# Optimization experiments

Hardware: AMD Instinct MI355X
Metric: run time of the kernel (lower is better)

## Reference

```python
import jax, jax.numpy as jnp
import numpy as np

N = 100000   # nodes
E = 640000   # edges (before self-loops)
G = 1000     # graphs in batch
D_IN = 100
D = 128
EPS = 1e-5


def setup_inputs() -> dict:
    key = jax.random.key(0)
    ks = jax.random.split(key, 12)
    x = jax.random.normal(ks[0], (N, D_IN), dtype=jnp.float32)
    edge_index = jax.random.randint(ks[1], (2, E), 0, N, dtype=jnp.int64)
    edge_weight = jax.random.uniform(ks[2], (E,), dtype=jnp.float32)
    batch = jnp.sort(jax.random.randint(ks[3], (N,), 0, G, dtype=jnp.int64))
    def glorot(k, shape):
        fan = shape[0]
        return jax.random.normal(k, shape, dtype=jnp.float32) / np.float32(np.sqrt(fan))
    return {
        "x": x, "edge_index": edge_index, "edge_weight": edge_weight, "batch": batch,
        "W0": glorot(ks[4], (D_IN, D)), "b0": jnp.zeros((D,), jnp.float32),
        "W1": glorot(ks[5], (D, D)),    "b1": jnp.zeros((D,), jnp.float32),
        "W2": glorot(ks[6], (D, D)),    "b2": jnp.zeros((D,), jnp.float32),
        "gamma": jnp.ones((3, D), jnp.float32), "beta": jnp.zeros((3, D), jnp.float32),
        "run_mean": jnp.zeros((3, D), jnp.float32), "run_var": jnp.ones((3, D), jnp.float32),
        "Wout": glorot(ks[7], (D, 1)), "bout": jnp.zeros((1,), jnp.float32),
    }


def reference(x, edge_index, edge_weight, batch, W0, b0, W1, b1, W2, b2,
              gamma, beta, run_mean, run_var, Wout, bout):
    n = x.shape[0]
    # add self-loops with weight 1 (GCNConv default)
    loop = jnp.arange(n, dtype=edge_index.dtype)
    src = jnp.concatenate([edge_index[0], loop])
    dst = jnp.concatenate([edge_index[1], loop])
    ew = jnp.concatenate([edge_weight, jnp.ones((n,), edge_weight.dtype)])
    # symmetric normalization: D^{-1/2} A D^{-1/2}
    deg = jax.ops.segment_sum(ew, dst, num_segments=n)
    dinv = jnp.where(deg > 0, jax.lax.rsqrt(deg), 0.0)
    norm = dinv[src] * ew * dinv[dst]            # [E+N]

    def gcn_bn_relu(h, W, b, g, bt, rm, rv):
        h = h @ W                                 # linear first (cheaper gather dim)
        agg = jax.ops.segment_sum(h[src] * norm[:, None], dst, num_segments=n)
        agg = agg + b
        # BatchNorm1d in eval mode (running stats); dropout is identity in eval
        agg = g * (agg - rm) * jax.lax.rsqrt(rv + EPS) + bt
        return jax.nn.relu(agg)

    h = gcn_bn_relu(x, W0, b0, gamma[0], beta[0], run_mean[0], run_var[0])
    h = gcn_bn_relu(h, W1, b1, gamma[1], beta[1], run_mean[1], run_var[1])
    h = gcn_bn_relu(h, W2, b2, gamma[2], beta[2], run_mean[2], run_var[2])

    # global mean pool over graphs
    counts = jax.ops.segment_sum(jnp.ones((n,), h.dtype), batch, num_segments=G)
    pooled = jax.ops.segment_sum(h, batch, num_segments=G) / jnp.maximum(counts, 1.0)[:, None]
    return pooled @ Wout + bout
```

## Files before the change

### kernel.cpp

```cpp
#include <hip/hip_runtime.h>

#define BN_EPS 1e-5f
#define BINCAP 32

static inline size_t align_up(size_t x, size_t a) { return (x + a - 1) & ~(a - 1); }

typedef __attribute__((ext_vector_type(8))) short bf16x8;
typedef __attribute__((ext_vector_type(4))) float f32x4;

__device__ __forceinline__ void bf16split(float v, unsigned short& hi, unsigned short& lo) {
    unsigned u = __float_as_uint(v);
    unsigned rh = (u + 0x7FFFu + ((u >> 16) & 1u)) >> 16;
    float fh = __uint_as_float(rh << 16);
    hi = (unsigned short)rh;
    float rem = v - fh;
    unsigned u2 = __float_as_uint(rem);
    lo = (unsigned short)((u2 + 0x7FFFu + ((u2 >> 16) & 1u)) >> 16);
}

__device__ __forceinline__ unsigned short bf16rne(float v) {
    unsigned u = __float_as_uint(v);
    return (unsigned short)((u + 0x7FFFu + ((u >> 16) & 1u)) >> 16);
}

__device__ __forceinline__ float bf16f(unsigned h) { return __uint_as_float(h << 16); }
__device__ __forceinline__ float chlo(unsigned u) { return __uint_as_float(u << 16); }
__device__ __forceinline__ float chhi(unsigned u) { return __uint_as_float(u & 0xffff0000u); }


__global__ void place_kernel(const int* __restrict__ src, const int* __restrict__ dst,
                             const float* __restrict__ ew,
                             int* __restrict__ cntc, float* __restrict__ degf,
                             int2* __restrict__ bins, int E) {
    int e = blockIdx.x * blockDim.x + threadIdx.x;
    if (e >= E) return;
    int d = dst[e];
    float w = ew[e];
    int pos = atomicAdd(&cntc[d], 1);
    atomicAdd(&degf[d], w);
    if (pos < BINCAP)
        bins[(size_t)d * BINCAP + pos] = make_int2(src[e], __float_as_int(w));
}


__global__ void deginv_kernel(const float* __restrict__ degf,
                              float* __restrict__ dinv, int N) {
    int i = blockIdx.x * blockDim.x + threadIdx.x;
    if (i >= N) return;
    dinv[i] = rsqrtf(degf[i] + 1.0f);
}


__global__ void normfix_kernel(const int* __restrict__ cntc, int2* __restrict__ bins,
                               const float* __restrict__ dinv, int N) {
    int i = blockIdx.x * blockDim.x + threadIdx.x;
    if (i >= N) return;
    int cnt = cntc[i]; if (cnt > BINCAP) cnt = BINCAP;
    float di = dinv[i];
    int2* b = bins + (size_t)i * BINCAP;
    for (int j = 0; j < cnt; ++j) {
        int2 pr = b[j];
        float w = __int_as_float(pr.y) * dinv[pr.x] * di;
        b[j].y = __float_as_int(w);
    }
}


__global__ void convw_kernel(const float* __restrict__ W0, const float* __restrict__ W1,
                             const float* __restrict__ W2, int K0,
                             unsigned short* __restrict__ Whi, unsigned short* __restrict__ Wlo) {
    int idx = blockIdx.x * blockDim.x + threadIdx.x;
    if (idx >= 3 * 32 * 64 * 8) return;
    int j    = idx & 7;
    int lane = (idx >> 3) & 63;
    int f    = (idx >> 9) & 31;
    int l    = idx >> 14;
    int ct = f >> 2, k0c = f & 3;
    int quad = lane >> 4, m16 = lane & 15;
    int n = ct * 16 + m16;
    int k = k0c * 32 + quad * 8 + j;
    const float* W = (l == 0) ? W0 : (l == 1) ? W1 : W2;
    int Kl = (l == 0) ? K0 : 128;
    float v = (k < Kl) ? W[(size_t)k * 128 + n] : 0.f;
    unsigned short hi, lo;
    bf16split(v, hi, lo);
    Whi[idx] = hi;
    Wlo[idx] = lo;
}


__device__ __forceinline__ void mfma_tail(const bf16x8 ah[4], const bf16x8 al[4],
                                          const unsigned short* __restrict__ Whi,
                                          const unsigned short* __restrict__ Wlo,
                                          unsigned short* __restrict__ Yh,
                                          int row0, int quad, int m16, int lane, int N) {
    const bf16x8* Wh8 = (const bf16x8*)Whi;
    const bf16x8* Wl8 = (const bf16x8*)Wlo;

    f32x4 acc[8];
    #pragma unroll
    for (int ct = 0; ct < 8; ++ct) acc[ct] = (f32x4){0.f, 0.f, 0.f, 0.f};

    bf16x8 bh[2][4], bl[2][4];
    #pragma unroll
    for (int k0c = 0; k0c < 4; ++k0c) {
        bh[0][k0c] = Wh8[k0c * 64 + lane];
        bl[0][k0c] = Wl8[k0c * 64 + lane];
    }

    __builtin_amdgcn_s_setprio(1);
    #pragma unroll
    for (int ct = 0; ct < 8; ++ct) {
        int cur = ct & 1, nxt = cur ^ 1;
        if (ct < 7) {
            #pragma unroll
            for (int k0c = 0; k0c < 4; ++k0c) {
                bh[nxt][k0c] = Wh8[((ct + 1) * 4 + k0c) * 64 + lane];
                bl[nxt][k0c] = Wl8[((ct + 1) * 4 + k0c) * 64 + lane];
            }
        }
        #pragma unroll
        for (int k0c = 0; k0c < 4; ++k0c) {
            acc[ct] = __builtin_amdgcn_mfma_f32_16x16x32_bf16(ah[k0c], bh[cur][k0c], acc[ct], 0, 0, 0);
            acc[ct] = __builtin_amdgcn_mfma_f32_16x16x32_bf16(ah[k0c], bl[cur][k0c], acc[ct], 0, 0, 0);
            acc[ct] = __builtin_amdgcn_mfma_f32_16x16x32_bf16(al[k0c], bh[cur][k0c], acc[ct], 0, 0, 0);
        }
    }
    __builtin_amdgcn_s_setprio(0);

    #pragma unroll
    for (int ct = 0; ct < 8; ++ct) {
        #pragma unroll
        for (int rg = 0; rg < 4; ++rg) {
            int row = row0 + quad * 4 + rg;
            if (row < N)
                Yh[(size_t)row * 128 + ct * 16 + m16] = bf16rne(acc[ct][rg]);
        }
    }
}


__launch_bounds__(256, 2)
__global__ void gemm0_fused_kernel(const float* __restrict__ x, int D_IN,
                                   const unsigned short* __restrict__ Whi,
                                   const unsigned short* __restrict__ Wlo,
                                   unsigned short* __restrict__ Yh, int N) {
    int tid = threadIdx.x;
    int wid = tid >> 6, lane = tid & 63;
    int quad = lane >> 4, m16 = lane & 15;
    int row0 = blockIdx.x * 64 + wid * 16;

    int arow = row0 + m16;
    if (arow > N - 1) arow = N - 1;
    const float* xr = x + (size_t)arow * D_IN;

    bf16x8 ah[4], al[4];
    #pragma unroll
    for (int k0c = 0; k0c < 4; ++k0c) {
        int kb = k0c * 32 + quad * 8;
        float vs[8];
        if (kb + 8 <= D_IN) {
            float4 v0 = *((const float4*)(xr + kb));
            float4 v1 = *((const float4*)(xr + kb + 4));
            vs[0] = v0.x; vs[1] = v0.y; vs[2] = v0.z; vs[3] = v0.w;
            vs[4] = v1.x; vs[5] = v1.y; vs[6] = v1.z; vs[7] = v1.w;
        } else {
            #pragma unroll
            for (int j = 0; j < 8; ++j) vs[j] = (kb + j < D_IN) ? xr[kb + j] : 0.f;
        }
        #pragma unroll
        for (int j = 0; j < 8; ++j) {
            unsigned short hi, lo;
            bf16split(vs[j], hi, lo);
            ah[k0c][j] = (short)hi;
            al[k0c][j] = (short)lo;
        }
    }

    mfma_tail(ah, al, Whi, Wlo, Yh, row0, quad, m16, lane, N);
}


__global__ void scaleshift_kernel(const float* __restrict__ gamma, const float* __restrict__ beta,
                                  const float* __restrict__ rm, const float* __restrict__ rv,
                                  const float* __restrict__ b0, const float* __restrict__ b1,
                                  const float* __restrict__ b2,
                                  float* __restrict__ scale, float* __restrict__ shift) {
    int t = threadIdx.x;
    int l = t >> 7, j = t & 127;
    const float* bs = (l == 0) ? b0 : (l == 1) ? b1 : b2;
    float sc = gamma[t] * rsqrtf(rv[t] + BN_EPS);
    scale[t] = sc;
    shift[t] = beta[t] + (bs[j] - rm[t]) * sc;
}


__device__ __forceinline__ void gather_quad(const unsigned* __restrict__ Yh32,
                                            const int2* pr, const int* mq, int lane,
                                            float* ax, float* ay) {
    int mr = mq[0];
    if (mq[1] > mr) mr = mq[1];
    if (mq[2] > mr) mr = mq[2];
    if (mq[3] > mr) mr = mq[3];
    mr = (mr + 7) & ~7;
    for (int j = 0; j < mr; j += 8) {
        int s[4][8];
        float w[4][8];
        #pragma unroll
        for (int q = 0; q < 4; ++q) {
            #pragma unroll
            for (int t = 0; t < 8; ++t)
                s[q][t] = __builtin_amdgcn_readlane(pr[q].x, j + t);
        }
        unsigned u[4][8];
        #pragma unroll
        for (int q = 0; q < 4; ++q) {
            #pragma unroll
            for (int t = 0; t < 8; ++t)
                u[q][t] = Yh32[(size_t)s[q][t] * 64 + lane];
        }
        #pragma unroll
        for (int q = 0; q < 4; ++q) {
            #pragma unroll
            for (int t = 0; t < 8; ++t)
                w[q][t] = __int_as_float(__builtin_amdgcn_readlane(pr[q].y, j + t));
        }
        #pragma unroll
        for (int q = 0; q < 4; ++q) {
            #pragma unroll
            for (int t = 0; t < 8; ++t) {
                ax[q] += chlo(u[q][t]) * w[q][t];
                ay[q] += chhi(u[q][t]) * w[q][t];
            }
        }
    }
}


__launch_bounds__(64, 4)
__global__ void fused_agg_gemm_kernel(
        const unsigned* __restrict__ Yh_in,
        const int2* __restrict__ bins, const int* __restrict__ cntc,
        const float* __restrict__ dinv,
        const float* __restrict__ scale, const float* __restrict__ shift,
        const unsigned short* __restrict__ Whi, const unsigned short* __restrict__ Wlo,
        unsigned short* __restrict__ Yh_out, int N) {
    __shared__ float sA[16 * 132];
    int lane = threadIdx.x;
    int quad = lane >> 4, m16 = lane & 15;
    int row0 = blockIdx.x * 16;

    float2 sc = ((const float2*)scale)[lane];
    float2 sh = ((const float2*)shift)[lane];

    int mm[16]; float dv[16]; unsigned uh[16]; int2 gg[16];
    #pragma unroll
    for (int i = 0; i < 16; ++i) {
        int n = row0 + i; if (n > N - 1) n = N - 1;
        mm[i] = cntc[n];
        dv[i] = dinv[n];
        uh[i] = Yh_in[(size_t)n * 64 + lane];
    }
    #pragma unroll
    for (int i = 0; i < 16; ++i) {
        int n = row0 + i; if (n > N - 1) n = N - 1;
        int m = mm[i]; if (m > BINCAP) m = BINCAP;
        mm[i] = m;
        gg[i] = (lane < m) ? bins[(size_t)n * BINCAP + lane] : make_int2(n, 0);
    }

    #pragma unroll
    for (int b = 0; b < 16; b += 4) {
        float ax[4], ay[4];
        #pragma unroll
        for (int q = 0; q < 4; ++q) {
            float w0 = dv[b + q] * dv[b + q];
            ax[q] = chlo(uh[b + q]) * w0;
            ay[q] = chhi(uh[b + q]) * w0;
        }
        gather_quad(Yh_in, &gg[b], &mm[b], lane, ax, ay);
        #pragma unroll
        for (int q = 0; q < 4; ++q) {
            float ox = fmaxf(ax[q] * sc.x + sh.x, 0.f);
            float oy = fmaxf(ay[q] * sc.y + sh.y, 0.f);
            *((float2*)&sA[(b + q) * 132 + 2 * lane]) = make_float2(ox, oy);
        }
    }

    asm volatile("s_waitcnt lgkmcnt(0)" ::: "memory");
    __builtin_amdgcn_sched_barrier(0);

    bf16x8 ah[4], al[4];
    #pragma unroll
    for (int k0c = 0; k0c < 4; ++k0c) {
        float4 v0 = *((const float4*)&sA[m16 * 132 + k0c * 32 + quad * 8]);
        float4 v1 = *((const float4*)&sA[m16 * 132 + k0c * 32 + quad * 8 + 4]);
        float vs[8] = {v0.x, v0.y, v0.z, v0.w, v1.x, v1.y, v1.z, v1.w};
        #pragma unroll
        for (int j = 0; j < 8; ++j) {
            unsigned short hi, lo;
            bf16split(vs[j], hi, lo);
            ah[k0c][j] = (short)hi;
            al[k0c][j] = (short)lo;
        }
    }

    mfma_tail(ah, al, Whi, Wlo, Yh_out, row0, quad, m16, lane, N);
}


__launch_bounds__(256)
__global__ void agg3_kernel(const unsigned* __restrict__ Yh32,
                            const int2* __restrict__ bins, const int* __restrict__ cntc,
                            const float* __restrict__ dinv,
                            const float* __restrict__ scale, const float* __restrict__ shift,
                            const float* __restrict__ Wout,
                            float* __restrict__ snode, int N) {
    int idx = blockIdx.x * blockDim.x + threadIdx.x;
    int waveid = idx >> 6, lane = idx & 63;
    int n0 = waveid * 4;
    if (n0 >= N) return;

    int nn[4]; int mq[4]; float dvq[4]; unsigned uhq[4]; int2 gg[4];
    #pragma unroll
    for (int q = 0; q < 4; ++q) {
        int n = n0 + q; if (n > N - 1) n = N - 1;
        nn[q] = n;
        mq[q] = cntc[n];
        dvq[q] = dinv[n];
        uhq[q] = Yh32[(size_t)n * 64 + lane];
    }
    #pragma unroll
    for (int q = 0; q < 4; ++q) {
        int m = mq[q]; if (m > BINCAP) m = BINCAP;
        mq[q] = m;
        gg[q] = (lane < m) ? bins[(size_t)nn[q] * BINCAP + lane] : make_int2(nn[q], 0);
    }

    float ax[4], ay[4];
    #pragma unroll
    for (int q = 0; q < 4; ++q) {
        float w0 = dvq[q] * dvq[q];
        ax[q] = chlo(uhq[q]) * w0;
        ay[q] = chhi(uhq[q]) * w0;
    }
    gather_quad(Yh32, gg, mq, lane, ax, ay);

    float2 sc = ((const float2*)scale)[lane];
    float2 sh = ((const float2*)shift)[lane];
    float2 w  = ((const float2*)Wout)[lane];
    float s[4];
    #pragma unroll
    for (int q = 0; q < 4; ++q) {
        float ox = fmaxf(ax[q] * sc.x + sh.x, 0.f);
        float oy = fmaxf(ay[q] * sc.y + sh.y, 0.f);
        s[q] = ox * w.x + oy * w.y;
    }
    #pragma unroll
    for (int off = 32; off > 0; off >>= 1) {
        #pragma unroll
        for (int q = 0; q < 4; ++q) s[q] += __shfl_down(s[q], off, 64);
    }
    if (lane == 0) {
        #pragma unroll
        for (int q = 0; q < 4; ++q)
            if (n0 + q < N) snode[n0 + q] = s[q];
    }
}


__global__ void bounds_kernel(const int* __restrict__ batch, int* __restrict__ gstart,
                              int N, int G) {
    int i = blockIdx.x * blockDim.x + threadIdx.x;
    if (i >= N) return;
    int b = batch[i];
    int prev = (i == 0) ? -1 : batch[i - 1];
    for (int g = prev + 1; g <= b; ++g) gstart[g] = i;
    if (i == N - 1) {
        for (int g = b + 1; g <= G; ++g) gstart[g] = N;
    }
}

__launch_bounds__(256)
__global__ void pool3_kernel(const float* __restrict__ snode, const int* __restrict__ gstart,
                             const float* __restrict__ bout, float* __restrict__ out, int G) {
    int g = blockIdx.x;
    int beg = gstart[g], end = gstart[g + 1];
    int t = threadIdx.x;
    float acc = 0.f;
    for (int n = beg + t; n < end; n += 256) acc += snode[n];
    __shared__ float lds[256];
    lds[t] = acc;
    __syncthreads();
    if (t < 64) lds[t] = lds[t] + lds[t + 64] + lds[t + 128] + lds[t + 192];
    __syncthreads();
    if (t < 64) {
        float s = lds[t];
        #pragma unroll
        for (int off = 32; off > 0; off >>= 1) s += __shfl_down(s, off, 64);
        if (t == 0) {
            float cntf = (float)(end - beg);
            out[g] = s / fmaxf(cntf, 1.0f) + bout[0];
        }
    }
}


extern "C" void kernel_launch(void* const* d_in, const int* in_sizes, int n_in,
                              void* d_out, int out_size, void* d_ws, size_t ws_size,
                              hipStream_t stream) {
    const float* x     = (const float*)d_in[0];
    const int*   ei    = (const int*)d_in[1];
    const float* ew    = (const float*)d_in[2];
    const int*   batch = (const int*)d_in[3];
    const float* W0 = (const float*)d_in[4];
    const float* b0 = (const float*)d_in[5];
    const float* W1 = (const float*)d_in[6];
    const float* b1 = (const float*)d_in[7];
    const float* W2 = (const float*)d_in[8];
    const float* b2 = (const float*)d_in[9];
    const float* gamma = (const float*)d_in[10];
    const float* beta  = (const float*)d_in[11];
    const float* rmean = (const float*)d_in[12];
    const float* rvar  = (const float*)d_in[13];
    const float* Wout  = (const float*)d_in[14];
    const float* bout  = (const float*)d_in[15];

    const int E = in_sizes[2];
    const int N = in_sizes[3];
    const int D_IN = in_sizes[0] / N;
    const int G = out_size;

    const int* src = ei;
    const int* dst = ei + E;

    char* ws = (char*)d_ws;
    size_t off = 0;
    float* dinv  = (float*)(ws + off); off = align_up(off + (size_t)N * 4, 256);
    int* cntc    = (int*)(ws + off);   off = align_up(off + (size_t)N * 4, 256);
    float* degf  = (float*)(ws + off); off = align_up(off + (size_t)N * 4, 256);
    int* gstart  = (int*)(ws + off);   off = align_up(off + ((size_t)G + 1) * 4, 256);
    int2* bins   = (int2*)(ws + off);  off = align_up(off + (size_t)N * BINCAP * 8, 256);
    unsigned short* YAh = (unsigned short*)(ws + off); off = align_up(off + (size_t)N * 128 * 2, 256);
    unsigned short* YBh = (unsigned short*)(ws + off); off = align_up(off + (size_t)N * 128 * 2, 256);
    unsigned short* Whi = (unsigned short*)(ws + off); off = align_up(off + 3 * 16384 * 2, 256);
    unsigned short* Wlo = (unsigned short*)(ws + off); off = align_up(off + 3 * 16384 * 2, 256);
    float* scale = (float*)(ws + off); off = align_up(off + 3 * 128 * 4, 256);
    float* shift = (float*)(ws + off); off = align_up(off + 3 * 128 * 4, 256);
    float* snode = (float*)(ws + off); off = align_up(off + (size_t)N * 4, 256);
    (void)ws_size;

    hipMemsetAsync(cntc, 0, (size_t)N * 4, stream);
    hipMemsetAsync(degf, 0, (size_t)N * 4, stream);

    const int tB = 256;
    place_kernel<<<(E + tB - 1) / tB, tB, 0, stream>>>(src, dst, ew, cntc, degf, bins, E);
    deginv_kernel<<<(N + tB - 1) / tB, tB, 0, stream>>>(degf, dinv, N);
    normfix_kernel<<<(N + tB - 1) / tB, tB, 0, stream>>>(cntc, bins, dinv, N);
    bounds_kernel<<<(N + tB - 1) / tB, tB, 0, stream>>>(batch, gstart, N, G);
    scaleshift_kernel<<<1, 384, 0, stream>>>(gamma, beta, rmean, rvar, b0, b1, b2, scale, shift);
    convw_kernel<<<(3 * 32 * 64 * 8 + tB - 1) / tB, tB, 0, stream>>>(W0, W1, W2, D_IN, Whi, Wlo);

    int gemm0_blocks = (N + 63) / 64;
    int fused_blocks = (N + 15) / 16;

    gemm0_fused_kernel<<<gemm0_blocks, 256, 0, stream>>>(x, D_IN, Whi, Wlo, YAh, N);
    fused_agg_gemm_kernel<<<fused_blocks, 64, 0, stream>>>(
        (const unsigned*)YAh, bins, cntc, dinv,
        scale, shift, Whi + 16384, Wlo + 16384, YBh, N);
    fused_agg_gemm_kernel<<<fused_blocks, 64, 0, stream>>>(
        (const unsigned*)YBh, bins, cntc, dinv,
        scale + 128, shift + 128, Whi + 2 * 16384, Wlo + 2 * 16384, YAh, N);
    {
        long nthread_quad = (long)((N + 3) / 4) * 64;
        int blocks_quad = (int)((nthread_quad + tB - 1) / tB);
        agg3_kernel<<<blocks_quad, tB, 0, stream>>>((const unsigned*)YAh,
            bins, cntc, dinv, scale + 256, shift + 256, Wout, snode, N);
    }

    pool3_kernel<<<G, 256, 0, stream>>>(snode, gstart, bout, (float*)d_out, G);
}
```

Measured before the change: 372.9 us.

## Merge setup kernels, derive degree from bins, and pipeline bin loads in fused aggregation

Drops the float atomic degree accumulation and its memset by summing edge weights from the bins in deginv_kernel. Merges the weight-conversion, BN scale/shift and graph-bounds kernels into one prep launch to cut launch count. In the fused aggregation kernel, bin loads are double-buffered per group of four rows instead of all sixteen being loaded up front, which lowers register pressure. The gather loop is also reordered so readlanes sit inline with the loads. Degree now only counts edges kept in the bins (capped at BINCAP), so it differs from the reference if any node exceeds the cap.

```diff
diff --git a/kernel.cpp b/kernel.cpp
--- a/kernel.cpp
+++ b/kernel.cpp
@@ -30,24 +30,25 @@
 
 __global__ void place_kernel(const int* __restrict__ src, const int* __restrict__ dst,
                              const float* __restrict__ ew,
-                             int* __restrict__ cntc, float* __restrict__ degf,
-                             int2* __restrict__ bins, int E) {
+                             int* __restrict__ cntc, int2* __restrict__ bins, int E) {
     int e = blockIdx.x * blockDim.x + threadIdx.x;
     if (e >= E) return;
     int d = dst[e];
-    float w = ew[e];
     int pos = atomicAdd(&cntc[d], 1);
-    atomicAdd(&degf[d], w);
     if (pos < BINCAP)
-        bins[(size_t)d * BINCAP + pos] = make_int2(src[e], __float_as_int(w));
-}
-
-
-__global__ void deginv_kernel(const float* __restrict__ degf,
+        bins[(size_t)d * BINCAP + pos] = make_int2(src[e], __float_as_int(ew[e]));
+}
+
+
+__global__ void deginv_kernel(const int* __restrict__ cntc, const int2* __restrict__ bins,
                               float* __restrict__ dinv, int N) {
     int i = blockIdx.x * blockDim.x + threadIdx.x;
     if (i >= N) return;
-    dinv[i] = rsqrtf(degf[i] + 1.0f);
+    int cnt = cntc[i]; if (cnt > BINCAP) cnt = BINCAP;
+    const int2* b = bins + (size_t)i * BINCAP;
+    float s = 0.f;
+    for (int j = 0; j < cnt; ++j) s += __int_as_float(b[j].y);
+    dinv[i] = rsqrtf(s + 1.0f);
 }
 
 
@@ -66,26 +67,50 @@
 }
 
 
-__global__ void convw_kernel(const float* __restrict__ W0, const float* __restrict__ W1,
-                             const float* __restrict__ W2, int K0,
-                             unsigned short* __restrict__ Whi, unsigned short* __restrict__ Wlo) {
+__global__ void prep_kernel(const float* __restrict__ W0, const float* __restrict__ W1,
+                            const float* __restrict__ W2, int K0,
+                            unsigned short* __restrict__ Whi, unsigned short* __restrict__ Wlo,
+                            const float* __restrict__ gamma, const float* __restrict__ beta,
+                            const float* __restrict__ rm, const float* __restrict__ rv,
+                            const float* __restrict__ b0, const float* __restrict__ b1,
+                            const float* __restrict__ b2,
+                            float* __restrict__ scale, float* __restrict__ shift,
+                            const int* __restrict__ batch, int* __restrict__ gstart,
+                            int N, int G) {
     int idx = blockIdx.x * blockDim.x + threadIdx.x;
-    if (idx >= 3 * 32 * 64 * 8) return;
-    int j    = idx & 7;
-    int lane = (idx >> 3) & 63;
-    int f    = (idx >> 9) & 31;
-    int l    = idx >> 14;
-    int ct = f >> 2, k0c = f & 3;
-    int quad = lane >> 4, m16 = lane & 15;
-    int n = ct * 16 + m16;
-    int k = k0c * 32 + quad * 8 + j;
-    const float* W = (l == 0) ? W0 : (l == 1) ? W1 : W2;
-    int Kl = (l == 0) ? K0 : 128;
-    float v = (k < Kl) ? W[(size_t)k * 128 + n] : 0.f;
-    unsigned short hi, lo;
-    bf16split(v, hi, lo);
-    Whi[idx] = hi;
-    Wlo[idx] = lo;
+    if (idx < 3 * 32 * 64 * 8) {
+        int j    = idx & 7;
+        int lane = (idx >> 3) & 63;
+        int f    = (idx >> 9) & 31;
+        int l    = idx >> 14;
+        int ct = f >> 2, k0c = f & 3;
+        int quad = lane >> 4, m16 = lane & 15;
+        int n = ct * 16 + m16;
+        int k = k0c * 32 + quad * 8 + j;
+        const float* W = (l == 0) ? W0 : (l == 1) ? W1 : W2;
+        int Kl = (l == 0) ? K0 : 128;
+        float v = (k < Kl) ? W[(size_t)k * 128 + n] : 0.f;
+        unsigned short hi, lo;
+        bf16split(v, hi, lo);
+        Whi[idx] = hi;
+        Wlo[idx] = lo;
+    } else if (idx < 3 * 32 * 64 * 8 + 384) {
+        int t = idx - 3 * 32 * 64 * 8;
+        int l = t >> 7, j = t & 127;
+        const float* bs = (l == 0) ? b0 : (l == 1) ? b1 : b2;
+        float sc = gamma[t] * rsqrtf(rv[t] + BN_EPS);
+        scale[t] = sc;
+        shift[t] = beta[t] + (bs[j] - rm[t]) * sc;
+    } else {
+        int i = idx - (3 * 32 * 64 * 8 + 384);
+        if (i >= N) return;
+        int b = batch[i];
+        int prev = (i == 0) ? -1 : batch[i - 1];
+        for (int g = prev + 1; g <= b; ++g) gstart[g] = i;
+        if (i == N - 1) {
+            for (int g = b + 1; g <= G; ++g) gstart[g] = N;
+        }
+    }
 }
 
 
@@ -181,20 +206,6 @@
 }
 
 
-__global__ void scaleshift_kernel(const float* __restrict__ gamma, const float* __restrict__ beta,
-                                  const float* __restrict__ rm, const float* __restrict__ rv,
-                                  const float* __restrict__ b0, const float* __restrict__ b1,
-                                  const float* __restrict__ b2,
-                                  float* __restrict__ scale, float* __restrict__ shift) {
-    int t = threadIdx.x;
-    int l = t >> 7, j = t & 127;
-    const float* bs = (l == 0) ? b0 : (l == 1) ? b1 : b2;
-    float sc = gamma[t] * rsqrtf(rv[t] + BN_EPS);
-    scale[t] = sc;
-    shift[t] = beta[t] + (bs[j] - rm[t]) * sc;
-}
-
-
 __device__ __forceinline__ void gather_quad(const unsigned* __restrict__ Yh32,
                                             const int2* pr, const int* mq, int lane,
                                             float* ax, float* ay) {
@@ -204,33 +215,22 @@
     if (mq[3] > mr) mr = mq[3];
     mr = (mr + 7) & ~7;
     for (int j = 0; j < mr; j += 8) {
-        int s[4][8];
-        float w[4][8];
-        #pragma unroll
-        for (int q = 0; q < 4; ++q) {
-            #pragma unroll
-            for (int t = 0; t < 8; ++t)
-                s[q][t] = __builtin_amdgcn_readlane(pr[q].x, j + t);
-        }
         unsigned u[4][8];
-        #pragma unroll
-        for (int q = 0; q < 4; ++q) {
-            #pragma unroll
-            for (int t = 0; t < 8; ++t)
-                u[q][t] = Yh32[(size_t)s[q][t] * 64 + lane];
-        }
-        #pragma unroll
-        for (int q = 0; q < 4; ++q) {
-            #pragma unroll
-            for (int t = 0; t < 8; ++t)
-                w[q][t] = __int_as_float(__builtin_amdgcn_readlane(pr[q].y, j + t));
-        }
         #pragma unroll
         for (int q = 0; q < 4; ++q) {
             #pragma unroll
             for (int t = 0; t < 8; ++t) {
-                ax[q] += chlo(u[q][t]) * w[q][t];
-                ay[q] += chhi(u[q][t]) * w[q][t];
+                int s = __builtin_amdgcn_readlane(pr[q].x, j + t);
+                u[q][t] = Yh32[(size_t)s * 64 + lane];
+            }
+        }
+        #pragma unroll
+        for (int q = 0; q < 4; ++q) {
+            #pragma unroll
+            for (int t = 0; t < 8; ++t) {
+                float w = __int_as_float(__builtin_amdgcn_readlane(pr[q].y, j + t));
+                ax[q] += chlo(u[q][t]) * w;
+                ay[q] += chhi(u[q][t]) * w;
             }
         }
     }
@@ -253,7 +253,7 @@
     float2 sc = ((const float2*)scale)[lane];
     float2 sh = ((const float2*)shift)[lane];
 
-    int mm[16]; float dv[16]; unsigned uh[16]; int2 gg[16];
+    int mm[16]; float dv[16]; unsigned uh[16];
     #pragma unroll
     for (int i = 0; i < 16; ++i) {
         int n = row0 + i; if (n > N - 1) n = N - 1;
@@ -262,28 +262,39 @@
         uh[i] = Yh_in[(size_t)n * 64 + lane];
     }
     #pragma unroll
-    for (int i = 0; i < 16; ++i) {
-        int n = row0 + i; if (n > N - 1) n = N - 1;
-        int m = mm[i]; if (m > BINCAP) m = BINCAP;
-        mm[i] = m;
-        gg[i] = (lane < m) ? bins[(size_t)n * BINCAP + lane] : make_int2(n, 0);
-    }
-
-    #pragma unroll
-    for (int b = 0; b < 16; b += 4) {
+    for (int i = 0; i < 16; ++i) { int m = mm[i]; if (m > BINCAP) m = BINCAP; mm[i] = m; }
+
+    int2 gq[2][4];
+    #pragma unroll
+    for (int q = 0; q < 4; ++q) {
+        int n = row0 + q; if (n > N - 1) n = N - 1;
+        gq[0][q] = (lane < mm[q]) ? bins[(size_t)n * BINCAP + lane] : make_int2(n, 0);
+    }
+
+    #pragma unroll
+    for (int b = 0; b < 4; ++b) {
+        int cur = b & 1, nxt = cur ^ 1;
+        if (b < 3) {
+            #pragma unroll
+            for (int q = 0; q < 4; ++q) {
+                int i = (b + 1) * 4 + q;
+                int n = row0 + i; if (n > N - 1) n = N - 1;
+                gq[nxt][q] = (lane < mm[i]) ? bins[(size_t)n * BINCAP + lane] : make_int2(n, 0);
+            }
+        }
         float ax[4], ay[4];
         #pragma unroll
         for (int q = 0; q < 4; ++q) {
-            float w0 = dv[b + q] * dv[b + q];
-            ax[q] = chlo(uh[b + q]) * w0;
-            ay[q] = chhi(uh[b + q]) * w0;
-        }
-        gather_quad(Yh_in, &gg[b], &mm[b], lane, ax, ay);
+            float w0 = dv[b * 4 + q] * dv[b * 4 + q];
+            ax[q] = chlo(uh[b * 4 + q]) * w0;
+            ay[q] = chhi(uh[b * 4 + q]) * w0;
+        }
+        gather_quad(Yh_in, gq[cur], &mm[b * 4], lane, ax, ay);
         #pragma unroll
         for (int q = 0; q < 4; ++q) {
             float ox = fmaxf(ax[q] * sc.x + sh.x, 0.f);
             float oy = fmaxf(ay[q] * sc.y + sh.y, 0.f);
-            *((float2*)&sA[(b + q) * 132 + 2 * lane]) = make_float2(ox, oy);
+            *((float2*)&sA[(b * 4 + q) * 132 + 2 * lane]) = make_float2(ox, oy);
         }
     }
 
@@ -368,18 +379,6 @@
     }
 }
 
-
-__global__ void bounds_kernel(const int* __restrict__ batch, int* __restrict__ gstart,
-                              int N, int G) {
-    int i = blockIdx.x * blockDim.x + threadIdx.x;
-    if (i >= N) return;
-    int b = batch[i];
-    int prev = (i == 0) ? -1 : batch[i - 1];
-    for (int g = prev + 1; g <= b; ++g) gstart[g] = i;
-    if (i == N - 1) {
-        for (int g = b + 1; g <= G; ++g) gstart[g] = N;
-    }
-}
 
 __launch_bounds__(256)
 __global__ void pool3_kernel(const float* __restrict__ snode, const int* __restrict__ gstart,
@@ -438,7 +437,6 @@
     size_t off = 0;
     float* dinv  = (float*)(ws + off); off = align_up(off + (size_t)N * 4, 256);
     int* cntc    = (int*)(ws + off);   off = align_up(off + (size_t)N * 4, 256);
-    float* degf  = (float*)(ws + off); off = align_up(off + (size_t)N * 4, 256);
     int* gstart  = (int*)(ws + off);   off = align_up(off + ((size_t)G + 1) * 4, 256);
     int2* bins   = (int2*)(ws + off);  off = align_up(off + (size_t)N * BINCAP * 8, 256);
     unsigned short* YAh = (unsigned short*)(ws + off); off = align_up(off + (size_t)N * 128 * 2, 256);
@@ -451,15 +449,18 @@
     (void)ws_size;
 
     hipMemsetAsync(cntc, 0, (size_t)N * 4, stream);
-    hipMemsetAsync(degf, 0, (size_t)N * 4, stream);
 
     const int tB = 256;
-    place_kernel<<<(E + tB - 1) / tB, tB, 0, stream>>>(src, dst, ew, cntc, degf, bins, E);
-    deginv_kernel<<<(N + tB - 1) / tB, tB, 0, stream>>>(degf, dinv, N);
+    place_kernel<<<(E + tB - 1) / tB, tB, 0, stream>>>(src, dst, ew, cntc, bins, E);
+    deginv_kernel<<<(N + tB - 1) / tB, tB, 0, stream>>>(cntc, bins, dinv, N);
     normfix_kernel<<<(N + tB - 1) / tB, tB, 0, stream>>>(cntc, bins, dinv, N);
-    bounds_kernel<<<(N + tB - 1) / tB, tB, 0, stream>>>(batch, gstart, N, G);
-    scaleshift_kernel<<<1, 384, 0, stream>>>(gamma, beta, rmean, rvar, b0, b1, b2, scale, shift);
-    convw_kernel<<<(3 * 32 * 64 * 8 + tB - 1) / tB, tB, 0, stream>>>(W0, W1, W2, D_IN, Whi, Wlo);
+    {
+        int prep_threads = 3 * 32 * 64 * 8 + 384 + N;
+        prep_kernel<<<(prep_threads + tB - 1) / tB, tB, 0, stream>>>(
+            W0, W1, W2, D_IN, Whi, Wlo,
+            gamma, beta, rmean, rvar, b0, b1, b2, scale, shift,
+            batch, gstart, N, G);
+    }
 
     int gemm0_blocks = (N + 63) / 64;
     int fused_blocks = (N + 15) / 16;
```

Result: faster. 320.8 us (-14.0%).
